# Kernel tuning notes

Measured on AMD Instinct MI355X. Metric: run time of the kernel, lower is better.

The kernel has to match this reference:

```python
import jax, jax.numpy as jnp
import numpy as np

BL = 512
Q_DIM = K_DIM = V_DIM = 512
R = 2
C = Q_DIM // R  # 256


def setup_inputs() -> dict:
    key = jax.random.key(0)
    ks = jax.random.split(key, 11)
    L = 32768
    x1 = jax.random.normal(ks[0], (1, Q_DIM, L), dtype=jnp.float32)
    x2 = jax.random.normal(ks[1], (1, Q_DIM, L), dtype=jnp.float32)
    mask = jnp.ones((1, 1, L), dtype=jnp.float32)
    s_in = 1.0 / np.sqrt(Q_DIM)
    s_out = 1.0 / np.sqrt(C)
    Wq = jax.random.normal(ks[2], (C, Q_DIM), dtype=jnp.float32) * s_in
    bq = jax.random.normal(ks[3], (C,), dtype=jnp.float32) * 0.01
    Wk = jax.random.normal(ks[4], (C, K_DIM), dtype=jnp.float32) * s_in
    bk = jax.random.normal(ks[5], (C,), dtype=jnp.float32) * 0.01
    Wv = jax.random.normal(ks[6], (C, V_DIM), dtype=jnp.float32) * s_in
    bv = jax.random.normal(ks[7], (C,), dtype=jnp.float32) * 0.01
    Wo = jax.random.normal(ks[8], (V_DIM, C), dtype=jnp.float32) * s_out
    bo = jax.random.normal(ks[9], (V_DIM,), dtype=jnp.float32) * 0.01
    return {"x1": x1, "x2": x2, "mask": mask, "Wq": Wq, "bq": bq,
            "Wk": Wk, "bk": bk, "Wv": Wv, "bv": bv, "Wo": Wo, "bo": bo}


def _sliding_att(x1, mask, Wq, bq, Wk, bk, Wv, bv, Wo, bo):
    bl = BL
    half = bl // 2
    B, _, L = x1.shape  # B == 1 (asserted in original)
    # 1x1 Conv1d projections == per-position matmuls over channels
    q = jnp.einsum('oc,bcl->bol', Wq, x1) + bq[None, :, None]  # (1,C,L)
    k = jnp.einsum('oc,bcl->bol', Wk, x1) + bk[None, :, None]
    v = jnp.einsum('oc,bcl->bol', Wv, x1) + bv[None, :, None]
    c1 = q.shape[1]
    nb = L // bl  # L chosen as multiple of bl; padding branch is a no-op
    pm = mask[:, 0:1, :]  # (1,1,L)
    # query blocks: (nb, C, bl)
    qb = q.reshape(1, c1, nb, bl).transpose(0, 2, 1, 3).reshape(nb, c1, bl)
    # pad K/V/mask with bl//2 zeros each side, gather overlapping windows of width 2*bl
    k_pad = jnp.pad(k, ((0, 0), (0, 0), (half, half)))[0]      # (C, L+bl)
    v_pad = jnp.pad(v, ((0, 0), (0, 0), (half, half)))[0]
    pm_pad = jnp.pad(pm, ((0, 0), (0, 0), (half, half)))[0, 0]  # (L+bl,)
    idx = jnp.arange(nb)[:, None] * bl + jnp.arange(2 * bl)[None, :]  # (nb, 2bl)
    kw = k_pad[:, idx].transpose(1, 0, 2)  # (nb, C, 2bl)
    vw = v_pad[:, idx].transpose(1, 0, 2)  # (nb, C, 2bl)
    pmw = pm_pad[idx][:, None, :]          # (nb, 1, 2bl)
    # banded window mask: query i attends keys j with i <= j < i+bl (in window coords)
    rows = jnp.arange(bl)[:, None]
    cols = jnp.arange(2 * bl)[None, :]
    wmask = ((cols >= rows) & (cols < rows + bl)).astype(x1.dtype)  # (bl, 2bl)
    fmask = wmask[None, :, :] * pmw  # (nb, bl, 2bl)
    scale = 1.0 / np.sqrt(c1)
    energy = jnp.einsum('ncl,ncm->nlm', qb, kw) * scale  # (nb, bl, 2bl)
    attn = jax.nn.softmax(energy + jnp.log(fmask + 1e-6), axis=-1) * fmask
    out = jnp.einsum('ncm,nlm->ncl', vw, attn)  # (nb, C, bl)
    out = jax.nn.relu(out)
    out = jnp.einsum('oc,ncl->nol', Wo, out) + bo[None, :, None]  # (nb, V, bl)
    out = out[None].transpose(0, 2, 1, 3).reshape(1, Wo.shape[0], nb * bl)
    return out[:, :, :L] * pm


def reference(x1, x2, mask, Wq, bq, Wk, bk, Wv, bv, Wo, bo):
    # x2 is accepted by the original forward but unused in self-attention
    return _sliding_att(x1, mask, Wq, bq, Wk, bk, Wv, bv, Wo, bo)
```

## Files before the change

### kernel.cpp

```cpp
#include <hip/hip_runtime.h>
#include <hip/hip_bf16.h>
#include <math.h>

#define L 32768
#define C 256
#define QD 512
#define SCALE (1.0f/16.0f)

typedef __hip_bfloat16 bf16;
typedef short v8s __attribute__((ext_vector_type(8)));
typedef short v4s __attribute__((ext_vector_type(4)));
typedef float v4f __attribute__((ext_vector_type(4)));
typedef float v16f __attribute__((ext_vector_type(16)));
typedef int   v4i __attribute__((ext_vector_type(4)));

__device__ __forceinline__ void ldst16(void* lds, const void* g) {
    __builtin_amdgcn_global_load_lds(
        (const __attribute__((address_space(1))) unsigned int*)g,
        (__attribute__((address_space(3))) unsigned int*)lds, 16, 0, 0);
}
__device__ __forceinline__ short bfbits(float x) {
    bf16 h = __float2bfloat16(x);
    return *reinterpret_cast<short*>(&h);
}
__device__ __forceinline__ int cvtpk(float lo, float hi) {
    int d;
    asm("v_cvt_pk_bf16_f32 %0, %1, %2" : "=v"(d) : "v"(lo), "v"(hi));
    return d;
}
__device__ __forceinline__ void pl32swap(int &x, int &y) {
    asm("v_permlane32_swap_b32 %0, %1" : "+v"(x), "+v"(y));
}

__global__ __launch_bounds__(256) void prep(
    const float* __restrict__ Wq, const float* __restrict__ Wk,
    const float* __restrict__ Wv, const float* __restrict__ bq,
    const float* __restrict__ bk, const float* __restrict__ bv,
    const float* __restrict__ Wo,
    bf16* __restrict__ Wall, bf16* __restrict__ Wob, float* __restrict__ ball)
{
    int i = blockIdx.x * 256 + threadIdx.x;
    if (i < 768*512) {
        int row = i >> 9, idx = i & 511;
        const float* src = row < 256 ? Wq : row < 512 ? Wk : Wv;
        float v = src[(row & 255) * 512 + idx];
        if (row < 256) v *= SCALE;
        Wall[i] = __float2bfloat16(v);
    } else if (i < 768*512 + 512*256) {
        int j = i - 768*512;
        Wob[j] = __float2bfloat16(Wo[j]);
    } else if (i < 768*512 + 512*256 + 768) {
        int j = i - 768*512 - 512*256;
        ball[j] = j < 256 ? bq[j]*SCALE : j < 512 ? bk[j - 256] : bv[j - 512];
    }
}

__global__ __launch_bounds__(256) void convt(
    const float* __restrict__ x, short* __restrict__ xT)
{
    __shared__ short st[64*72];
    const int t = threadIdx.x;
    const int l0 = blockIdx.x * 64, c0 = blockIdx.y * 64;
    #pragma unroll
    for (int i = 0; i < 2; i++) {
        int v = i*256 + t;
        int c = v >> 3, l8 = (v & 7) << 3;
        const float* p = x + (size_t)(c0 + c) * L + l0 + l8;
        float4 f0 = *(const float4*)p;
        float4 f1 = *(const float4*)(p + 4);
        bf16* stb = (bf16*)st;
        stb[(l8+0)*72 + c] = __float2bfloat16(f0.x);
        stb[(l8+1)*72 + c] = __float2bfloat16(f0.y);
        stb[(l8+2)*72 + c] = __float2bfloat16(f0.z);
        stb[(l8+3)*72 + c] = __float2bfloat16(f0.w);
        stb[(l8+4)*72 + c] = __float2bfloat16(f1.x);
        stb[(l8+5)*72 + c] = __float2bfloat16(f1.y);
        stb[(l8+6)*72 + c] = __float2bfloat16(f1.z);
        stb[(l8+7)*72 + c] = __float2bfloat16(f1.w);
    }
    __syncthreads();
    #pragma unroll
    for (int i = 0; i < 2; i++) {
        int v = i*256 + t;
        int l = v >> 3, c8 = (v & 7) << 3;
        *(v8s*)(xT + (size_t)(l0 + l) * QD + c0 + c8) = *(const v8s*)&st[l*72 + c8];
    }
}

__global__ __launch_bounds__(256) void qkv_gemm(
    const bf16* __restrict__ A, const bf16* __restrict__ B,
    const float* __restrict__ ball,
    bf16* __restrict__ qT, bf16* __restrict__ kT, bf16* __restrict__ vB)
{
    __shared__ short sA[128*32];
    __shared__ short sB[128*32];
    __shared__ short sE[128*136];

    const int t    = threadIdx.x;
    const int lane = t & 63;
    const int w    = t >> 6;
    const int wm   = w & 1, wn = w >> 1;
    const int col  = lane & 15, quad = lane >> 4;
    const int n0   = blockIdx.x * 128;
    const int my   = blockIdx.y;
    const int m0   = my * 128;

    v4f acc[4][4];
    #pragma unroll
    for (int i = 0; i < 4; i++)
        #pragma unroll
        for (int j = 0; j < 4; j++) acc[i][j] = (v4f){0.f,0.f,0.f,0.f};

    for (int k0 = 0; k0 < QD; k0 += 32) {
        #pragma unroll
        for (int j = 0; j < 2; j++) {
            int idx = j*256 + t;
            int m = idx >> 2, k8 = (idx & 3) << 3;
            ldst16(&sA[idx*8], A + (size_t)(m0 + m) * QD + k0 + k8);
        }
        #pragma unroll
        for (int j = 0; j < 2; j++) {
            int idx = j*256 + t;
            int n = idx >> 2, k8 = (idx & 3) << 3;
            ldst16(&sB[idx*8], B + (size_t)(n0 + n) * QD + k0 + k8);
        }
        __syncthreads();
        v8s af[4], bf[4];
        #pragma unroll
        for (int mt = 0; mt < 4; mt++)
            af[mt] = *(const v8s*)&sA[(wm*64 + mt*16 + col)*32 + quad*8];
        #pragma unroll
        for (int nt = 0; nt < 4; nt++)
            bf[nt] = *(const v8s*)&sB[(wn*64 + nt*16 + col)*32 + quad*8];
        #pragma unroll
        for (int mt = 0; mt < 4; mt++)
            #pragma unroll
            for (int nt = 0; nt < 4; nt++)
                acc[mt][nt] = __builtin_amdgcn_mfma_f32_16x16x32_bf16(af[mt], bf[nt], acc[mt][nt], 0, 0, 0);
        __syncthreads();
    }

    float bias_v[4][4];
    #pragma unroll
    for (int mt = 0; mt < 4; mt++)
        #pragma unroll
        for (int r = 0; r < 4; r++)
            bias_v[mt][r] = ball[m0 + wm*64 + mt*16 + quad*4 + r];

    bf16* sEb = (bf16*)sE;
    if (my < 4) {
        #pragma unroll
        for (int mt = 0; mt < 4; mt++)
            #pragma unroll
            for (int nt = 0; nt < 4; nt++)
                #pragma unroll
                for (int r = 0; r < 4; r++)
                    sEb[(wn*64 + nt*16 + col)*136 + wm*64 + mt*16 + quad*4 + r] =
                        __float2bfloat16(acc[mt][nt][r] + bias_v[mt][r]);
        __syncthreads();
        bf16* dst = (my < 2) ? qT : kT;
        const int c0 = (my & 1) * 128;
        #pragma unroll
        for (int j = 0; j < 8; j++) {
            int idx = j*256 + t;
            int n = idx >> 4, c8 = (idx & 15) << 3;
            *(v8s*)(dst + (size_t)(n0 + n) * C + c0 + c8) = *(const v8s*)&sE[n*136 + c8];
        }
    } else {
        #pragma unroll
        for (int mt = 0; mt < 4; mt++)
            #pragma unroll
            for (int nt = 0; nt < 4; nt++)
                #pragma unroll
                for (int r = 0; r < 4; r++)
                    sEb[(wm*64 + mt*16 + quad*4 + r)*136 + wn*64 + nt*16 + col] =
                        __float2bfloat16(acc[mt][nt][r] + bias_v[mt][r]);
        __syncthreads();
        const int c0 = (my - 4) * 128;
        #pragma unroll
        for (int j = 0; j < 8; j++) {
            int idx = j*256 + t;
            int m = idx >> 4, n8 = (idx & 15) << 3;
            *(v8s*)(vB + (size_t)(c0 + m) * L + n0 + n8) = *(const v8s*)&sE[m*136 + n8];
        }
    }
}

__global__ __launch_bounds__(256) void out_gemm(
    const bf16* __restrict__ A, const bf16* __restrict__ B,
    const float* __restrict__ bo, const float* __restrict__ mask,
    float* __restrict__ out)
{
    __shared__ short sA[128*32];
    __shared__ short sB[128*32];
    __shared__ float sEf[64*132];

    const int t    = threadIdx.x;
    const int lane = t & 63;
    const int w    = t >> 6;
    const int wm   = w & 1, wn = w >> 1;
    const int col  = lane & 15, quad = lane >> 4;
    const int n0   = blockIdx.x * 128;
    const int m0   = blockIdx.y * 128;

    v4f acc[4][4];
    #pragma unroll
    for (int i = 0; i < 4; i++)
        #pragma unroll
        for (int j = 0; j < 4; j++) acc[i][j] = (v4f){0.f,0.f,0.f,0.f};

    for (int k0 = 0; k0 < C; k0 += 32) {
        #pragma unroll
        for (int j = 0; j < 2; j++) {
            int idx = j*256 + t;
            int m = idx >> 2, k8 = (idx & 3) << 3;
            ldst16(&sA[idx*8], A + (size_t)(m0 + m) * C + k0 + k8);
        }
        #pragma unroll
        for (int j = 0; j < 2; j++) {
            int idx = j*256 + t;
            int n = idx >> 2, k8 = (idx & 3) << 3;
            ldst16(&sB[idx*8], B + (size_t)(n0 + n) * C + k0 + k8);
        }
        __syncthreads();
        v8s af[4], bf[4];
        #pragma unroll
        for (int mt = 0; mt < 4; mt++)
            af[mt] = *(const v8s*)&sA[(wm*64 + mt*16 + col)*32 + quad*8];
        #pragma unroll
        for (int nt = 0; nt < 4; nt++)
            bf[nt] = *(const v8s*)&sB[(wn*64 + nt*16 + col)*32 + quad*8];
        #pragma unroll
        for (int mt = 0; mt < 4; mt++)
            #pragma unroll
            for (int nt = 0; nt < 4; nt++)
                acc[mt][nt] = __builtin_amdgcn_mfma_f32_16x16x32_bf16(af[mt], bf[nt], acc[mt][nt], 0, 0, 0);
        __syncthreads();
    }

    #pragma unroll
    for (int half = 0; half < 2; half++) {
        if (wm == half) {
            #pragma unroll
            for (int mt = 0; mt < 4; mt++) {
                #pragma unroll
                for (int r = 0; r < 4; r++) {
                    float bb = bo[m0 + half*64 + mt*16 + quad*4 + r];
                    #pragma unroll
                    for (int nt = 0; nt < 4; nt++)
                        sEf[(mt*16 + quad*4 + r)*132 + wn*64 + nt*16 + col] =
                            acc[mt][nt][r] + bb;
                }
            }
        }
        __syncthreads();
        #pragma unroll
        for (int j = 0; j < 8; j++) {
            int idx = j*256 + t;
            int row = idx >> 5, s4 = (idx & 31) << 2;
            float4 vv = *(const float4*)&sEf[row*132 + s4];
            float4 mk = *(const float4*)&mask[n0 + s4];
            vv.x *= mk.x; vv.y *= mk.y; vv.z *= mk.z; vv.w *= mk.w;
            *(float4*)&out[(size_t)(m0 + half*64 + row) * L + n0 + s4] = vv;
        }
        __syncthreads();
    }
}

__device__ __forceinline__ void stage_kv(
    const short* __restrict__ kT, const short* __restrict__ vB,
    int a0, int t, short* __restrict__ sK, short* __restrict__ sV)
{
    #pragma unroll
    for (int i = 0; i < 9; i++) {
        int idx = i*256 + t;
        if (idx < 2112) {
            int row = idx / 33, s = idx % 33;
            int a  = min(max(a0 + row, 0), L - 1);
            int ss = min(s, 31);
            ldst16(&sK[idx*8], kT + (size_t)a * C + ss*8);
        }
    }
    #pragma unroll
    for (int i = 0; i < 8; i++) {
        int idx = i*256 + t;
        int row = idx >> 3, s = idx & 7;
        int sl  = s ^ (row & 7);
        int ab  = min(max(a0 + sl*8, 0), L - 8);
        ldst16(&sV[idx*8], vB + (size_t)row * L + ab);
    }
}

__global__ __launch_bounds__(256, 1) void attn_mfma(
    const bf16* __restrict__ qT, const bf16* __restrict__ kT,
    const bf16* __restrict__ vB, const float* __restrict__ mask,
    bf16* __restrict__ aoT)
{
    __shared__ short sK [2][64*264];
    __shared__ short sVt[2][256*64];

    const int t    = threadIdx.x;
    const int w    = t >> 6;
    const int lane = t & 63;
    const int l31  = lane & 31;
    const int hi   = lane >> 5;
    const int bx   = blockIdx.x;
    const int tile = ((bx & 7) << 5) | (bx >> 3);
    const int p0   = tile * 128;
    const int abase = p0 - 256;
    const int qg   = p0 + w*32 + l31;

    const short* kTs = (const short*)kT;
    const short* vBs = (const short*)vB;
    const short* qTs = (const short*)qT;

    stage_kv(kTs, vBs, abase, t, sK[0], sVt[0]);

    unsigned mb[10];
    #pragma unroll
    for (int ch = 0; ch < 10; ch++) {
        unsigned m = 0;
        int a0 = abase + ch*64;
        #pragma unroll
        for (int kt = 0; kt < 2; kt++) {
            #pragma unroll
            for (int b = 0; b < 4; b++) {
                int a4 = a0 + kt*32 + b*8 + hi*4;
                int ac = min(max(a4, 0), L - 4);
                float4 mv = *(const float4*)&mask[ac];
                float mvv[4] = {mv.x, mv.y, mv.z, mv.w};
                #pragma unroll
                for (int c = 0; c < 4; c++) {
                    int a   = a4 + c;
                    int rel = a - qg + 256;
                    bool ok = ((unsigned)rel < 512u) &&
                              ((unsigned)a < (unsigned)L) && (mvv[c] > 0.f);
                    if (ok) m |= (1u << (kt*16 + b*4 + c));
                }
            }
        }
        mb[ch] = m;
    }

    v16f oacc[8];
    #pragma unroll
    for (int i = 0; i < 8; i++)
        #pragma unroll
        for (int j = 0; j < 16; j++) oacc[i][j] = 0.f;
    float mrow = -1e30f, lrow = 0.f;

    int voff[4];
    #pragma unroll
    for (int j = 0; j < 4; j++) voff[j] = ((2*j + hi) ^ (l31 & 7)) * 8;

    __syncthreads();

    #pragma unroll
    for (int ch = 0; ch < 10; ch++) {
        const short* sKc = sK[ch & 1];
        const short* sVc = sVt[ch & 1];

        int qoff = 0;
        asm volatile("" : "+v"(qoff));
        const short* qp = qTs + (size_t)qg * C + hi*8 + qoff;
        v8s qfr[16];
        #pragma unroll
        for (int ks = 0; ks < 16; ks++) qfr[ks] = *(const v8s*)(qp + ks*16);

        if (ch < 9)
            stage_kv(kTs, vBs, abase + (ch+1)*64, t, sK[(ch+1)&1], sVt[(ch+1)&1]);

        #pragma unroll
        for (int kt = 0; kt < 2; kt++) {
            const short* kb = sKc + l31*264 + hi*8 + kt*8448;
            v16f e;
            #pragma unroll
            for (int j = 0; j < 16; j++) e[j] = 0.f;
            __builtin_amdgcn_s_setprio(1);
            #pragma unroll
            for (int ks = 0; ks < 16; ks++) {
                v8s af = *(const v8s*)(kb + ks*16);
                e = __builtin_amdgcn_mfma_f32_32x32x16_bf16(af, qfr[ks], e, 0, 0, 0);
            }
            __builtin_amdgcn_s_setprio(0);

            unsigned mbits = mb[ch] >> (kt*16);
            float cmax = -1e30f;
            #pragma unroll
            for (int r = 0; r < 16; r++) {
                bool ok = (mbits >> r) & 1;
                float x = ok ? e[r] : -1e30f;
                e[r] = x;
                cmax = fmaxf(cmax, x);
            }
            cmax = fmaxf(cmax, __shfl_xor(cmax, 32));

            if (cmax > mrow + 8.f) {
                float al = __expf(mrow - cmax);
                mrow = cmax;
                lrow *= al;
                #pragma unroll
                for (int i = 0; i < 8; i++)
                    #pragma unroll
                    for (int j = 0; j < 16; j++) oacc[i][j] *= al;
            }

            float psum = 0.f;
            #pragma unroll
            for (int r = 0; r < 16; r++) {
                float p = __expf(e[r] - mrow);
                e[r] = p;
                psum += p;
            }
            psum += __shfl_xor(psum, 32);
            lrow += psum;

            v8s pfr[2];
            #pragma unroll
            for (int g = 0; g < 2; g++) {
                int X = cvtpk(e[8*g+0], e[8*g+1]);
                int Y = cvtpk(e[8*g+2], e[8*g+3]);
                int U = cvtpk(e[8*g+4], e[8*g+5]);
                int V = cvtpk(e[8*g+6], e[8*g+7]);
                pl32swap(X, U);
                pl32swap(Y, V);
                v4i d = (v4i){X, Y, U, V};
                pfr[g] = *reinterpret_cast<v8s*>(&d);
            }

            const short* vb = sVc + l31*64;
            __builtin_amdgcn_s_setprio(1);
            #pragma unroll
            for (int cht = 0; cht < 8; cht++) {
                #pragma unroll
                for (int mf = 0; mf < 2; mf++) {
                    v8s vf = *(const v8s*)(vb + cht*2048 + voff[kt*2 + mf]);
                    oacc[cht] = __builtin_amdgcn_mfma_f32_32x32x16_bf16(
                        vf, pfr[mf], oacc[cht], 0, 0, 0);
                }
            }
            __builtin_amdgcn_s_setprio(0);
        }

        if (ch < 9) __syncthreads();
    }

    float inv = (lrow > 0.f) ? 1.f / lrow : 0.f;
    short* aorow = (short*)aoT + (size_t)qg * C;
    #pragma unroll
    for (int cht = 0; cht < 8; cht++) {
        #pragma unroll
        for (int b = 0; b < 4; b++) {
            v4s pk;
            #pragma unroll
            for (int c = 0; c < 4; c++)
                pk[c] = bfbits(fmaxf(oacc[cht][b*4 + c] * inv, 0.f));
            *(v4s*)(aorow + cht*32 + b*8 + hi*4) = pk;
        }
    }
}

extern "C" void kernel_launch(void* const* d_in, const int* in_sizes, int n_in,
                              void* d_out, int out_size, void* d_ws, size_t ws_size,
                              hipStream_t stream)
{
    const float* x1   = (const float*)d_in[0];
    const float* mask = (const float*)d_in[2];
    const float* Wq   = (const float*)d_in[3];
    const float* bq   = (const float*)d_in[4];
    const float* Wk   = (const float*)d_in[5];
    const float* bk   = (const float*)d_in[6];
    const float* Wv   = (const float*)d_in[7];
    const float* bv   = (const float*)d_in[8];
    const float* Wo   = (const float*)d_in[9];
    const float* bo   = (const float*)d_in[10];
    float* out = (float*)d_out;

    bf16* x1T  = (bf16*)d_ws;
    bf16* Wall = x1T + (size_t)L * QD;
    bf16* Wob  = Wall + 768*512;
    float* ball = (float*)(Wob + 512*256);
    bf16* qT   = (bf16*)(ball + 768);
    bf16* kT   = qT + (size_t)L * C;
    bf16* vB   = kT + (size_t)L * C;
    bf16* aoT  = vB + (size_t)L * C;

    dim3 blk(256);
    prep<<<dim3((768*512 + 512*256 + 768 + 255)/256), blk, 0, stream>>>(
        Wq, Wk, Wv, bq, bk, bv, Wo, Wall, Wob, ball);
    convt<<<dim3(L/64, QD/64), blk, 0, stream>>>(x1, (short*)x1T);
    qkv_gemm<<<dim3(L/128, 6), blk, 0, stream>>>(Wall, x1T, ball, qT, kT, vB);
    attn_mfma<<<dim3(L/128), dim3(256), 0, stream>>>(qT, kT, vB, mask, aoT);
    out_gemm<<<dim3(L/128, 4), blk, 0, stream>>>(Wob, aoT, bo, mask, out);
}
```

Baseline: 354.6 us.

## Split attention output channels across wave pairs with 512-thread blocks

The attention kernel now launches 512 threads per block. Each pair of waves shares a 32-query group, and each wave of the pair accumulates half of the 256 output channels, so the per-wave accumulator shrinks from 8 to 4 MFMA tiles. Q fragments are loaded once before the loop and kept in registers instead of being reloaded every chunk, and K/V staging is spread across the larger thread count. In exchange the QK^T MFMAs and the softmax work are done twice, once by each wave of a pair, while register pressure drops and more waves are available to hide latency.

```diff
diff --git a/kernel.cpp b/kernel.cpp
--- a/kernel.cpp
+++ b/kernel.cpp
@@ -272,8 +272,8 @@
     int a0, int t, short* __restrict__ sK, short* __restrict__ sV)
 {
     #pragma unroll
-    for (int i = 0; i < 9; i++) {
-        int idx = i*256 + t;
+    for (int i = 0; i < 5; i++) {
+        int idx = i*512 + t;
         if (idx < 2112) {
             int row = idx / 33, s = idx % 33;
             int a  = min(max(a0 + row, 0), L - 1);
@@ -282,8 +282,8 @@
         }
     }
     #pragma unroll
-    for (int i = 0; i < 8; i++) {
-        int idx = i*256 + t;
+    for (int i = 0; i < 4; i++) {
+        int idx = i*512 + t;
         int row = idx >> 3, s = idx & 7;
         int sl  = s ^ (row & 7);
         int ab  = min(max(a0 + sl*8, 0), L - 8);
@@ -291,7 +291,7 @@
     }
 }
 
-__global__ __launch_bounds__(256, 1) void attn_mfma(
+__global__ __launch_bounds__(512, 1) void attn_mfma(
     const bf16* __restrict__ qT, const bf16* __restrict__ kT,
     const bf16* __restrict__ vB, const float* __restrict__ mask,
     bf16* __restrict__ aoT)
@@ -301,6 +301,8 @@
 
     const int t    = threadIdx.x;
     const int w    = t >> 6;
+    const int qgrp = w >> 1;
+    const int dh   = w & 1;
     const int lane = t & 63;
     const int l31  = lane & 31;
     const int hi   = lane >> 5;
@@ -308,13 +310,20 @@
     const int tile = ((bx & 7) << 5) | (bx >> 3);
     const int p0   = tile * 128;
     const int abase = p0 - 256;
-    const int qg   = p0 + w*32 + l31;
+    const int qg   = p0 + qgrp*32 + l31;
 
     const short* kTs = (const short*)kT;
     const short* vBs = (const short*)vB;
     const short* qTs = (const short*)qT;
 
     stage_kv(kTs, vBs, abase, t, sK[0], sVt[0]);
+
+    v8s qf[16];
+    {
+        const short* qp = qTs + (size_t)qg * C + hi*8;
+        #pragma unroll
+        for (int ks = 0; ks < 16; ks++) qf[ks] = *(const v8s*)(qp + ks*16);
+    }
 
     unsigned mb[10];
     #pragma unroll
@@ -342,9 +351,9 @@
         mb[ch] = m;
     }
 
-    v16f oacc[8];
-    #pragma unroll
-    for (int i = 0; i < 8; i++)
+    v16f oacc[4];
+    #pragma unroll
+    for (int i = 0; i < 4; i++)
         #pragma unroll
         for (int j = 0; j < 16; j++) oacc[i][j] = 0.f;
     float mrow = -1e30f, lrow = 0.f;
@@ -359,14 +368,6 @@
     for (int ch = 0; ch < 10; ch++) {
         const short* sKc = sK[ch & 1];
         const short* sVc = sVt[ch & 1];
-
-        int qoff = 0;
-        asm volatile("" : "+v"(qoff));
-        const short* qp = qTs + (size_t)qg * C + hi*8 + qoff;
-        v8s qfr[16];
-        #pragma unroll
-        for (int ks = 0; ks < 16; ks++) qfr[ks] = *(const v8s*)(qp + ks*16);
-
         if (ch < 9)
             stage_kv(kTs, vBs, abase + (ch+1)*64, t, sK[(ch+1)&1], sVt[(ch+1)&1]);
 
@@ -380,7 +381,7 @@
             #pragma unroll
             for (int ks = 0; ks < 16; ks++) {
                 v8s af = *(const v8s*)(kb + ks*16);
-                e = __builtin_amdgcn_mfma_f32_32x32x16_bf16(af, qfr[ks], e, 0, 0, 0);
+                e = __builtin_amdgcn_mfma_f32_32x32x16_bf16(af, qf[ks], e, 0, 0, 0);
             }
             __builtin_amdgcn_s_setprio(0);
 
@@ -400,7 +401,7 @@
                 mrow = cmax;
                 lrow *= al;
                 #pragma unroll
-                for (int i = 0; i < 8; i++)
+                for (int i = 0; i < 4; i++)
                     #pragma unroll
                     for (int j = 0; j < 16; j++) oacc[i][j] *= al;
             }
@@ -428,15 +429,15 @@
                 pfr[g] = *reinterpret_cast<v8s*>(&d);
             }
 
-            const short* vb = sVc + l31*64;
+            const short* vb = sVc + l31*64 + dh*4*2048;
             __builtin_amdgcn_s_setprio(1);
             #pragma unroll
-            for (int cht = 0; cht < 8; cht++) {
+            for (int cl = 0; cl < 4; cl++) {
                 #pragma unroll
                 for (int mf = 0; mf < 2; mf++) {
-                    v8s vf = *(const v8s*)(vb + cht*2048 + voff[kt*2 + mf]);
-                    oacc[cht] = __builtin_amdgcn_mfma_f32_32x32x16_bf16(
-                        vf, pfr[mf], oacc[cht], 0, 0, 0);
+                    v8s vf = *(const v8s*)(vb + cl*2048 + voff[kt*2 + mf]);
+                    oacc[cl] = __builtin_amdgcn_mfma_f32_32x32x16_bf16(
+                        vf, pfr[mf], oacc[cl], 0, 0, 0);
                 }
             }
             __builtin_amdgcn_s_setprio(0);
@@ -448,14 +449,14 @@
     float inv = (lrow > 0.f) ? 1.f / lrow : 0.f;
     short* aorow = (short*)aoT + (size_t)qg * C;
     #pragma unroll
-    for (int cht = 0; cht < 8; cht++) {
+    for (int cl = 0; cl < 4; cl++) {
         #pragma unroll
         for (int b = 0; b < 4; b++) {
             v4s pk;
             #pragma unroll
             for (int c = 0; c < 4; c++)
-                pk[c] = bfbits(fmaxf(oacc[cht][b*4 + c] * inv, 0.f));
-            *(v4s*)(aorow + cht*32 + b*8 + hi*4) = pk;
+                pk[c] = bfbits(fmaxf(oacc[cl][b*4 + c] * inv, 0.f));
+            *(v4s*)(aorow + (dh*4 + cl)*32 + b*8 + hi*4) = pk;
         }
     }
 }
@@ -490,6 +491,6 @@
         Wq, Wk, Wv, bq, bk, bv, Wo, Wall, Wob, ball);
     convt<<<dim3(L/64, QD/64), blk, 0, stream>>>(x1, (short*)x1T);
     qkv_gemm<<<dim3(L/128, 6), blk, 0, stream>>>(Wall, x1T, ball, qT, kT, vB);
-    attn_mfma<<<dim3(L/128), dim3(256), 0, stream>>>(qT, kT, vB, mask, aoT);
+    attn_mfma<<<dim3(L/128), dim3(512), 0, stream>>>(qT, kT, vB, mask, aoT);
     out_gemm<<<dim3(L/128, 4), blk, 0, stream>>>(Wob, aoT, bo, mask, out);
 }
```

Measured after the change: 435.0 us. 1.23x slower.
